# Kernel optimization log

Measured on AMD Instinct MI355X. Metric: run time of the kernel, lower is better.

Reference implementation:

```python
import jax, jax.numpy as jnp
import numpy as np

N_NODES = 50000

def _sage_conv(x, src, dst, W_l, b_l, W_r):
    # mean-aggregate neighbor features: messages x[src] summed into dst
    msgs = x[src]                                   # [E, d]
    agg = jax.ops.segment_sum(msgs, dst, num_segments=N_NODES)  # [N, d]
    ones = jnp.ones((src.shape[0],), dtype=x.dtype)
    cnt = jax.ops.segment_sum(ones, dst, num_segments=N_NODES)  # [N]
    agg = agg / jnp.maximum(cnt, 1.0)[:, None]
    return agg @ W_l + b_l + x @ W_r


def setup_inputs() -> dict:
    key = jax.random.key(0)
    ks = jax.random.split(key, 8)
    d_in, hid, out = 64, 128, 64
    x = jax.random.normal(ks[0], (N_NODES, d_in), dtype=jnp.float32)
    edge_index = jax.random.randint(ks[1], (2, 1600000), 0, N_NODES, dtype=jnp.int64)
    def w(k, a, b):
        return jax.random.normal(k, (a, b), dtype=jnp.float32) / np.sqrt(a)
    return {
        "x": x,
        "edge_index": edge_index,
        "W_l1": w(ks[2], d_in, hid), "b_l1": jnp.zeros((hid,), jnp.float32),
        "W_r1": w(ks[3], d_in, hid),
        "W_l2": w(ks[4], hid, hid), "b_l2": jnp.zeros((hid,), jnp.float32),
        "W_r2": w(ks[5], hid, hid),
        "W_out": w(ks[6], hid, out), "b_out": jnp.zeros((out,), jnp.float32),
    }


def reference(x, edge_index, W_l1, b_l1, W_r1, W_l2, b_l2, W_r2, W_out, b_out):
    src, dst = edge_index[0], edge_index[1]
    h = jax.nn.relu(_sage_conv(x, src, dst, W_l1, b_l1, W_r1))
    h = jax.nn.relu(_sage_conv(h, src, dst, W_l2, b_l2, W_r2))
    return h @ W_out + b_out
```

## Files before the change

### kernel.cpp

```cpp
#include <hip/hip_runtime.h>


typedef unsigned short ushort_t;
typedef unsigned int uint_t;
typedef unsigned char uchar_t;
typedef __attribute__((ext_vector_type(8))) short short8;
typedef __attribute__((ext_vector_type(8))) ushort_t ushort8;
typedef __attribute__((ext_vector_type(4))) float f32x4;

#define BKT_SHIFT 7
#define BKT_NODES 128
#define BKT_CAP   5120
#define EPB       4096
#define QSCALE    32.0f
#define QINV      0.03125f
#define XQSCALE   16.0f

__device__ inline ushort_t bf16_rne(float v) {
    uint_t u = __float_as_uint(v);
    u += 0x7fffu + ((u >> 16) & 1u);
    return (ushort_t)(u >> 16);
}
__device__ inline float bf16_to_f(ushort_t h) {
    return __uint_as_float((uint_t)h << 16);
}


struct WPack {
    const float* srcp[5];
    ushort_t* dstp[5];
    int K[5], N[5], beg[5], end[5];
};

__global__ __launch_bounds__(1024)
void k_work(const int* __restrict__ src, const int* __restrict__ dst,
            uint_t* __restrict__ pairs, int* __restrict__ bcnt, int E, int nbk,
            int bbl, const float* __restrict__ x, ushort_t* __restrict__ xh,
            ushort_t* __restrict__ xl, uchar_t* __restrict__ xq,
            int NS, WPack wp, int total) {
    int tid = threadIdx.x;
    if (blockIdx.x >= bbl) {
        int t = (blockIdx.x - bbl) * 1024 + tid;
        if (t < NS) {
            float v = x[t];
            ushort_t h = bf16_rne(v);
            xh[t] = h;
            xl[t] = bf16_rne(v - bf16_to_f(h));
            int qv = (int)(v * XQSCALE + 128.5f);
            qv = qv < 0 ? 0 : (qv > 255 ? 255 : qv);
            xq[t] = (uchar_t)qv;
            return;
        }
        t -= NS;
        if (t >= total) return;
#pragma unroll
        for (int m = 0; m < 5; ++m) {
            if (t >= wp.beg[m] && t < wp.end[m]) {
                int i = t - wp.beg[m];
                int K = wp.K[m], N = wp.N[m];
                int k = i / N, nn = i % N;
                int NT = N >> 4;
                int kt = k >> 5, bq = (k >> 3) & 3, j = k & 7;
                int nt = nn >> 4, lane = (bq << 4) | (nn & 15);
                int base = (((kt * NT + nt) << 6) + lane) * 8 + j;
                int halfsz = (K >> 5) * NT * 512;
                float v = wp.srcp[m][i];
                ushort_t h = bf16_rne(v);
                wp.dstp[m][base] = h;
                wp.dstp[m][halfsz + base] = bf16_rne(v - bf16_to_f(h));
            }
        }
        return;
    }

    __shared__ int h[4][512];
    int sub = tid & 3;
    for (int i = tid; i < 4 * 512; i += 1024) ((int*)h)[i] = 0;
    __syncthreads();

    int e = blockIdx.x * EPB + tid * 4;
    bool full = (e + 4 <= E);
    int4 d4 = {0, 0, 0, 0}, s4 = {0, 0, 0, 0};
    if (full) {
        d4 = *(const int4*)(dst + e);
        s4 = *(const int4*)(src + e);
        atomicAdd(&h[sub][d4.x >> BKT_SHIFT], 1);
        atomicAdd(&h[sub][d4.y >> BKT_SHIFT], 1);
        atomicAdd(&h[sub][d4.z >> BKT_SHIFT], 1);
        atomicAdd(&h[sub][d4.w >> BKT_SHIFT], 1);
    } else {
        for (int t = e; t < E && t < e + 4; ++t)
            atomicAdd(&h[sub][dst[t] >> BKT_SHIFT], 1);
    }
    __syncthreads();
    for (int i = tid; i < nbk; i += 1024) {
        int c0 = h[0][i], c1 = h[1][i], c2 = h[2][i], c3 = h[3][i];
        int c = c0 + c1 + c2 + c3;
        int bs = c ? atomicAdd(&bcnt[i], c) : 0;
        h[0][i] = bs; h[1][i] = bs + c0; h[2][i] = bs + c0 + c1;
        h[3][i] = bs + c0 + c1 + c2;
    }
    __syncthreads();
    if (full) {
        int dd[4] = {d4.x, d4.y, d4.z, d4.w};
        int ss[4] = {s4.x, s4.y, s4.z, s4.w};
#pragma unroll
        for (int t = 0; t < 4; ++t) {
            int b = dd[t] >> BKT_SHIFT;
            int r = atomicAdd(&h[sub][b], 1);
            pairs[(size_t)b * BKT_CAP + r] =
                (uint_t)(ss[t] & 0xFFFF) | ((uint_t)(dd[t] & (BKT_NODES - 1)) << 16);
        }
    } else {
        for (int t = e; t < E && t < e + 4; ++t) {
            int d = dst[t];
            int b = d >> BKT_SHIFT;
            int r = atomicAdd(&h[sub][b], 1);
            pairs[(size_t)b * BKT_CAP + r] =
                (uint_t)(src[t] & 0xFFFF) | ((uint_t)(d & (BKT_NODES - 1)) << 16);
        }
    }
}


__global__ __launch_bounds__(1024) void k_csr(const uint_t* __restrict__ pairs,
                                              const int* __restrict__ bcnt,
                                              int* __restrict__ off,
                                              ushort_t* __restrict__ col, int n) {
    __shared__ int hist[BKT_NODES];
    __shared__ int s[BKT_NODES];
    __shared__ int cur[BKT_NODES];
    __shared__ int bofs_s;
    int b = blockIdx.x, tid = threadIdx.x;
    if (tid < 64) {
        int p = 0;
        for (int i = tid; i < b; i += 64) p += bcnt[i];
#pragma unroll
        for (int m = 1; m < 64; m <<= 1) p += __shfl_xor(p, m);
        if (tid == 0) bofs_s = p;
    }
    if (tid < BKT_NODES) hist[tid] = 0;
    __syncthreads();
    int bofs = bofs_s;
    int cnt = bcnt[b];
    const uint_t* p = pairs + (size_t)b * BKT_CAP;
    for (int i = tid; i < cnt; i += 1024) atomicAdd(&hist[(p[i] >> 16) & 127], 1);
    __syncthreads();
    int v = (tid < BKT_NODES) ? hist[tid] : 0;
    if (tid < BKT_NODES) s[tid] = v;
    __syncthreads();
    for (int ofs = 1; ofs < BKT_NODES; ofs <<= 1) {
        int t = (tid >= ofs && tid < BKT_NODES) ? s[tid - ofs] : 0;
        __syncthreads();
        if (tid < BKT_NODES) s[tid] += t;
        __syncthreads();
    }
    if (tid < BKT_NODES) {
        int excl = bofs + s[tid] - v;
        int node = b * BKT_NODES + tid;
        if (node <= n) off[node] = excl;
        cur[tid] = excl;
    }
    __syncthreads();
    for (int i = tid; i < cnt; i += 1024) {
        uint_t pk = p[i];
        int pos = atomicAdd(&cur[(pk >> 16) & 127], 1);
        col[pos] = (ushort_t)(pk & 0xFFFF);
    }
}

template <int ROWB>
__device__ inline void gather_u8(const uchar_t* __restrict__ fbase,
                                 const ushort_t* __restrict__ col,
                                 int s0, int s1, int sub,
                                 uint_t (&ae)[4], uint_t (&ao)[4]) {
    constexpr int EPI = 1024 / ROWB;
#pragma unroll
    for (int i = 0; i < 4; ++i) { ae[i] = 0u; ao[i] = 0u; }
    int e = s0;
    for (; e + 4 * EPI <= s1; e += 4 * EPI) {
        int c[4];
        uint4 q[4];
#pragma unroll
        for (int j = 0; j < 4; ++j) c[j] = col[e + j * EPI + sub];
#pragma unroll
        for (int j = 0; j < 4; ++j) q[j] = *(const uint4*)(fbase + (size_t)c[j] * ROWB);
#pragma unroll
        for (int j = 0; j < 4; ++j) {
            const uint_t* u = (const uint_t*)&q[j];
#pragma unroll
            for (int i = 0; i < 4; ++i) {
                ae[i] += u[i] & 0x00FF00FFu;
                ao[i] += (u[i] >> 8) & 0x00FF00FFu;
            }
        }
    }
    for (; e < s1; e += 2 * EPI) {
        int last = s1 - 1;
        int c[2];
        uint_t msk[2];
        uint4 q[2];
#pragma unroll
        for (int j = 0; j < 2; ++j) {
            int idx = e + j * EPI + sub;
            msk[j] = (idx < s1) ? 0xFFFFFFFFu : 0u;
            c[j] = col[min(idx, last)];
        }
#pragma unroll
        for (int j = 0; j < 2; ++j) q[j] = *(const uint4*)(fbase + (size_t)c[j] * ROWB);
#pragma unroll
        for (int j = 0; j < 2; ++j) {
            const uint_t* u = (const uint_t*)&q[j];
#pragma unroll
            for (int i = 0; i < 4; ++i) {
                uint_t um = u[i] & msk[j];
                ae[i] += um & 0x00FF00FFu;
                ao[i] += (um >> 8) & 0x00FF00FFu;
            }
        }
    }
}

__device__ inline f32x4 mfma3(f32x4 acc, short8 ah, short8 al, short8 bh, short8 bl) {
    acc = __builtin_amdgcn_mfma_f32_16x16x32_bf16(ah, bh, acc, 0, 0, 0);
    acc = __builtin_amdgcn_mfma_f32_16x16x32_bf16(al, bh, acc, 0, 0, 0);
    acc = __builtin_amdgcn_mfma_f32_16x16x32_bf16(ah, bl, acc, 0, 0, 0);
    return acc;
}


__global__ __launch_bounds__(512)
void k_layer1(const uchar_t* __restrict__ xq, const ushort_t* __restrict__ xh,
              const ushort_t* __restrict__ xl,
              const int* __restrict__ off, const ushort_t* __restrict__ col,
              const ushort_t* __restrict__ Wlp, const ushort_t* __restrict__ Wrp,
              const float* __restrict__ bias, ushort_t* __restrict__ Oh,
              uchar_t* __restrict__ OqA, uchar_t* __restrict__ OqB, int n) {
    __shared__ ushort_t Ahs[32][72];
    __shared__ ushort_t Als[32][72];
    int tid = threadIdx.x, waveid = tid >> 6, lane = tid & 63;
    int base = blockIdx.x * 32;
    int li = lane & 3;
    int sub = lane >> 2;
    const uchar_t* fbase = xq + li * 16;

    for (int q = 0; q < 4; ++q) {
        int node = base + waveid * 4 + q;
        int nd = node < n ? node : n - 1;
        int s0 = off[nd], s1 = off[nd + 1];
        uint_t ae[4], ao[4];
        gather_u8<64>(fbase, col, s0, s1, sub, ae, ao);
#pragma unroll
        for (int m = 4; m < 64; m <<= 1) {
#pragma unroll
            for (int i = 0; i < 4; ++i) {
                ae[i] += __shfl_xor(ae[i], m);
                ao[i] += __shfl_xor(ao[i], m);
            }
        }
        if (sub == 0) {
            int deg = s1 - s0;
            float inv = 1.f / (XQSCALE * fmaxf((float)deg, 1.f));
            float c8 = deg > 0 ? 8.f : 0.f;
            ushort_t vh[16], vl[16];
#pragma unroll
            for (int i = 0; i < 4; ++i) {
                uint_t f[4] = {ae[i] & 0xFFFFu, ao[i] & 0xFFFFu,
                               ae[i] >> 16, ao[i] >> 16};
#pragma unroll
                for (int b = 0; b < 4; ++b) {
                    float mval = (float)f[b] * inv - c8;
                    ushort_t h = bf16_rne(mval);
                    vh[i * 4 + b] = h;
                    vl[i * 4 + b] = bf16_rne(mval - bf16_to_f(h));
                }
            }
            int r = waveid * 4 + q;
            *(ushort8*)&Ahs[r][li * 16] = *(ushort8*)&vh[0];
            *(ushort8*)&Ahs[r][li * 16 + 8] = *(ushort8*)&vh[8];
            *(ushort8*)&Als[r][li * 16] = *(ushort8*)&vl[0];
            *(ushort8*)&Als[r][li * 16 + 8] = *(ushort8*)&vl[8];
        }
    }
    __syncthreads();

    int rowt = waveid >> 2, c0 = waveid & 3;
    int colq = lane & 15, quad = lane >> 4;
    int arow = rowt * 16 + colq;
    short8 fah[2], fal[2], fxh[2], fxl[2];
#pragma unroll
    for (int kt = 0; kt < 2; ++kt) {
        fah[kt] = *(const short8*)&Ahs[arow][kt * 32 + quad * 8];
        fal[kt] = *(const short8*)&Als[arow][kt * 32 + quad * 8];
    }
    int grow = base + arow; if (grow >= n) grow = n - 1;
#pragma unroll
    for (int kt = 0; kt < 2; ++kt) {
        fxh[kt] = *(const short8*)(xh + (size_t)grow * 64 + kt * 32 + quad * 8);
        fxl[kt] = *(const short8*)(xl + (size_t)grow * 64 + kt * 32 + quad * 8);
    }
#pragma unroll
    for (int t = 0; t < 2; ++t) {
        int nt = c0 + t * 4;
        float bv = bias[nt * 16 + colq];
        f32x4 acc = (f32x4){bv, bv, bv, bv};
#pragma unroll
        for (int kt = 0; kt < 2; ++kt) {
            const ushort_t* pL = Wlp + ((size_t)((kt * 8 + nt) << 6) + lane) * 8;
            acc = mfma3(acc, fah[kt], fal[kt],
                        *(const short8*)pL, *(const short8*)(pL + 8192));
            const ushort_t* pR = Wrp + ((size_t)((kt * 8 + nt) << 6) + lane) * 8;
            acc = mfma3(acc, fxh[kt], fxl[kt],
                        *(const short8*)pR, *(const short8*)(pR + 8192));
        }
        int rowb = base + rowt * 16 + quad * 4;
        int cix = nt * 16 + colq;
        uchar_t* Oqh = t ? OqB : OqA;
        int qix = c0 * 16 + colq;
#pragma unroll
        for (int r = 0; r < 4; ++r) {
            int row = rowb + r;
            if (row < n) {
                float v = fmaxf(acc[r], 0.f);
                Oh[(size_t)row * 128 + cix] = bf16_rne(v);
                int qv = (int)(v * QSCALE + 0.5f);
                Oqh[(size_t)row * 64 + qix] = (uchar_t)(qv > 255 ? 255 : qv);
            }
        }
    }
}


__global__ __launch_bounds__(256)
void k_aggh(const uchar_t* __restrict__ fq, const int* __restrict__ off,
            const ushort_t* __restrict__ col, uint_t* __restrict__ S, int n) {
    int wave = (int)((blockIdx.x * (unsigned)blockDim.x + threadIdx.x) >> 6);
    int lane = threadIdx.x & 63;
    if (wave >= n) return;
    int li = lane & 3, sub = lane >> 2;
    int s0 = off[wave], s1 = off[wave + 1];
    uint_t ae[4], ao[4];
    gather_u8<64>(fq + li * 16, col, s0, s1, sub, ae, ao);
#pragma unroll
    for (int m = 4; m < 64; m <<= 1) {
#pragma unroll
        for (int i = 0; i < 4; ++i) {
            ae[i] += __shfl_xor(ae[i], m);
            ao[i] += __shfl_xor(ao[i], m);
        }
    }
    if (sub == 0) {
        uint4 va = {ae[0], ae[1], ae[2], ae[3]};
        uint4 vo = {ao[0], ao[1], ao[2], ao[3]};
        *(uint4*)(S + (size_t)wave * 32 + li * 8) = va;
        *(uint4*)(S + (size_t)wave * 32 + li * 8 + 4) = vo;
    }
}


#define L2R 136
__global__ __launch_bounds__(256)
void k_dense2(const uint_t* __restrict__ SA, const uint_t* __restrict__ SB,
              const int* __restrict__ off, const ushort_t* __restrict__ h1h,
              const ushort_t* __restrict__ Wlp, const ushort_t* __restrict__ Wrp,
              const float* __restrict__ b2, const ushort_t* __restrict__ Wop,
              const float* __restrict__ bo, float* __restrict__ out, int n) {
    __shared__ ushort_t Ah[16][L2R], Al[16][L2R];
    __shared__ ushort_t Hh[16][L2R], Hl[16][L2R];
    int tid = threadIdx.x, waveid = tid >> 6, lane = tid & 63;
    int base = blockIdx.x * 16;

    int j = lane & 31;
    const uint_t* Sp = (lane < 32) ? SA : SB;
    int fofs = (lane < 32) ? 0 : 64;
    int fl = fofs + ((j >> 3) << 4) + ((j & 3) << 2) + ((j >> 2) & 1);
    for (int q = 0; q < 4; ++q) {
        int node = base + waveid * 4 + q;
        int nd = node < n ? node : n - 1;
        float inv = QINV / fmaxf((float)(off[nd + 1] - off[nd]), 1.f);
        uint_t s = Sp[(size_t)nd * 32 + j];
        float v0 = (float)(s & 0xFFFFu) * inv;
        float v1 = (float)(s >> 16) * inv;
        ushort_t h0 = bf16_rne(v0), h1v = bf16_rne(v1);
        int row = waveid * 4 + q;
        Ah[row][fl] = h0;      Al[row][fl] = bf16_rne(v0 - bf16_to_f(h0));
        Ah[row][fl + 2] = h1v; Al[row][fl + 2] = bf16_rne(v1 - bf16_to_f(h1v));
    }
    __syncthreads();

    int colx = lane & 15, quad = lane >> 4;
    int arow = colx;
    int grow = base + arow; if (grow >= n) grow = n - 1;
    short8 gah[4], gal[4], sh[4];
#pragma unroll
    for (int kt = 0; kt < 4; ++kt) {
        gah[kt] = *(const short8*)&Ah[arow][kt * 32 + quad * 8];
        gal[kt] = *(const short8*)&Al[arow][kt * 32 + quad * 8];
        sh[kt]  = *(const short8*)(h1h + (size_t)grow * 128 + kt * 32 + quad * 8);
    }
#pragma unroll
    for (int t = 0; t < 2; ++t) {
        int nt = waveid + t * 4;
        float bv = b2[nt * 16 + colx];
        f32x4 acc = (f32x4){bv, bv, bv, bv};
#pragma unroll
        for (int kt = 0; kt < 4; ++kt) {
            const ushort_t* pL = Wlp + ((size_t)((kt * 8 + nt) << 6) + lane) * 8;
            acc = mfma3(acc, gah[kt], gal[kt],
                        *(const short8*)pL, *(const short8*)(pL + 16384));
            const ushort_t* pR = Wrp + ((size_t)((kt * 8 + nt) << 6) + lane) * 8;
            short8 bh = *(const short8*)pR;
            short8 bl = *(const short8*)(pR + 16384);
            acc = __builtin_amdgcn_mfma_f32_16x16x32_bf16(sh[kt], bh, acc, 0, 0, 0);
            acc = __builtin_amdgcn_mfma_f32_16x16x32_bf16(sh[kt], bl, acc, 0, 0, 0);
        }
#pragma unroll
        for (int r = 0; r < 4; ++r) {
            int row = quad * 4 + r;
            float v = fmaxf(acc[r], 0.f);
            ushort_t h = bf16_rne(v);
            Hh[row][nt * 16 + colx] = h;
            Hl[row][nt * 16 + colx] = bf16_rne(v - bf16_to_f(h));
        }
    }
    __syncthreads();

    short8 hh[4], hl[4];
#pragma unroll
    for (int kt = 0; kt < 4; ++kt) {
        hh[kt] = *(const short8*)&Hh[arow][kt * 32 + quad * 8];
        hl[kt] = *(const short8*)&Hl[arow][kt * 32 + quad * 8];
    }
    int nt2 = waveid;
    float bv = bo[nt2 * 16 + colx];
    f32x4 acc2 = (f32x4){bv, bv, bv, bv};
#pragma unroll
    for (int kt = 0; kt < 4; ++kt) {
        const ushort_t* p = Wop + ((size_t)((kt * 4 + nt2) << 6) + lane) * 8;
        acc2 = mfma3(acc2, hh[kt], hl[kt],
                     *(const short8*)p, *(const short8*)(p + 8192));
    }
#pragma unroll
    for (int r = 0; r < 4; ++r) {
        int row = base + quad * 4 + r;
        if (row < n) out[(size_t)row * 64 + nt2 * 16 + colx] = acc2[r];
    }
}


static inline size_t align256(size_t x) { return (x + 255) & ~(size_t)255; }

extern "C" void kernel_launch(void* const* d_in, const int* in_sizes, int n_in,
                              void* d_out, int out_size, void* d_ws, size_t ws_size,
                              hipStream_t stream) {
    const float* x   = (const float*)d_in[0];
    const int*   ei  = (const int*)d_in[1];
    const float* Wl1 = (const float*)d_in[2];
    const float* bl1 = (const float*)d_in[3];
    const float* Wr1 = (const float*)d_in[4];
    const float* Wl2 = (const float*)d_in[5];
    const float* bl2 = (const float*)d_in[6];
    const float* Wr2 = (const float*)d_in[7];
    const float* Wo  = (const float*)d_in[8];
    const float* bo  = (const float*)d_in[9];

    const int N = in_sizes[0] / 64;
    const int E = in_sizes[1] / 2;
    const int* src = ei;
    const int* dst = ei + E;
    const int nbk = (N + BKT_NODES - 1) >> BKT_SHIFT;

    char* ws = (char*)d_ws;
    int* off = (int*)ws;            ws += align256((size_t)(N + 1) * 4);
    int* bcnt = (int*)ws;           ws += align256((size_t)nbk * 4);
    uint_t* pairs = (uint_t*)ws;    ws += align256((size_t)nbk * BKT_CAP * 4);
    ushort_t* col = (ushort_t*)ws;  ws += align256((size_t)E * 2);
    ushort_t* xh  = (ushort_t*)ws;  ws += align256((size_t)N * 64 * 2);
    ushort_t* xl  = (ushort_t*)ws;  ws += align256((size_t)N * 64 * 2);
    uchar_t*  xq  = (uchar_t*)ws;   ws += align256((size_t)N * 64);
    ushort_t* h1h = (ushort_t*)ws;  ws += align256((size_t)N * 128 * 2);
    uchar_t*  h1qA = (uchar_t*)ws;  ws += align256((size_t)N * 64);
    uchar_t*  h1qB = (uchar_t*)ws;  ws += align256((size_t)N * 64);
    uint_t*   SA  = (uint_t*)ws;    ws += align256((size_t)N * 32 * 4);
    uint_t*   SB  = (uint_t*)ws;    ws += align256((size_t)N * 32 * 4);
    ushort_t* Wl1p = (ushort_t*)ws; ws += align256((size_t)2 * 64 * 128 * 2);
    ushort_t* Wr1p = (ushort_t*)ws; ws += align256((size_t)2 * 64 * 128 * 2);
    ushort_t* Wl2p = (ushort_t*)ws; ws += align256((size_t)2 * 128 * 128 * 2);
    ushort_t* Wr2p = (ushort_t*)ws; ws += align256((size_t)2 * 128 * 128 * 2);
    ushort_t* Wop  = (ushort_t*)ws; ws += align256((size_t)2 * 128 * 64 * 2);

    WPack wp;
    wp.srcp[0] = Wl1; wp.dstp[0] = Wl1p; wp.K[0] = 64;  wp.N[0] = 128;
    wp.srcp[1] = Wr1; wp.dstp[1] = Wr1p; wp.K[1] = 64;  wp.N[1] = 128;
    wp.srcp[2] = Wl2; wp.dstp[2] = Wl2p; wp.K[2] = 128; wp.N[2] = 128;
    wp.srcp[3] = Wr2; wp.dstp[3] = Wr2p; wp.K[3] = 128; wp.N[3] = 128;
    wp.srcp[4] = Wo;  wp.dstp[4] = Wop;  wp.K[4] = 128; wp.N[4] = 64;
    int acc_el = 0;
    for (int m = 0; m < 5; ++m) {
        wp.beg[m] = acc_el; acc_el += wp.K[m] * wp.N[m]; wp.end[m] = acc_el;
    }
    int NS = N * 64;

    hipMemsetAsync(bcnt, 0, (size_t)nbk * 4, stream);
    int bbl = (E + EPB - 1) / EPB;
    int pbl = (NS + acc_el + 1023) / 1024;
    k_work<<<bbl + pbl, 1024, 0, stream>>>(src, dst, pairs, bcnt, E, nbk, bbl,
                                           x, xh, xl, xq, NS, wp, acc_el);

    k_csr<<<nbk, 1024, 0, stream>>>(pairs, bcnt, off, col, N);

    k_layer1<<<(N + 31) / 32, 512, 0, stream>>>(xq, xh, xl, off, col, Wl1p,
                                                Wr1p, bl1, h1h, h1qA, h1qB, N);

    int aggbl = (N * 64 + 255) / 256;
    k_aggh<<<aggbl, 256, 0, stream>>>(h1qA, off, col, SA, N);
    k_aggh<<<aggbl, 256, 0, stream>>>(h1qB, off, col, SB, N);

    k_dense2<<<(N + 15) / 16, 256, 0, stream>>>(SA, SB, off, h1h, Wl2p, Wr2p,
                                                bl2, Wop, bo, (float*)d_out, N);
}
```

Measured before the change: 233.0 us.

## Replace CSR build with bucket-local LDS atomic aggregation fused into dense layers

Drops the CSR construction kernel and the separate per-node gather and aggregation kernels. Each 64-node bucket block now reads its unsorted (src,dst) pairs directly, accumulates quantized neighbor features into shared memory with atomics, then runs the dense MFMA stages in the same block. This cuts the launch count from six kernels to three and removes the off/col/SA/SB intermediate traffic. The cost is heavy LDS atomic contention and only about 782 blocks of 1024 threads, so occupancy may be low. Bucket capacity shrinks to 2816 edges per bucket, which risks overflow on skewed graphs.

After: 236.8 us. Within noise of the previous version (+1.6%).

```diff
diff --git a/kernel.cpp b/kernel.cpp
--- a/kernel.cpp
+++ b/kernel.cpp
@@ -8,9 +8,9 @@
 typedef __attribute__((ext_vector_type(8))) ushort_t ushort8;
 typedef __attribute__((ext_vector_type(4))) float f32x4;
 
-#define BKT_SHIFT 7
-#define BKT_NODES 128
-#define BKT_CAP   5120
+#define BKT_SHIFT 6
+#define BKT_NODES 64
+#define BKT_CAP   2816
 #define EPB       4096
 #define QSCALE    32.0f
 #define QINV      0.03125f
@@ -73,9 +73,9 @@
         return;
     }
 
-    __shared__ int h[4][512];
+    __shared__ int h[4][1024];
     int sub = tid & 3;
-    for (int i = tid; i < 4 * 512; i += 1024) ((int*)h)[i] = 0;
+    for (int i = tid; i < 4 * 1024; i += 1024) ((int*)h)[i] = 0;
     __syncthreads();
 
     int e = blockIdx.x * EPB + tid * 4;
@@ -122,105 +122,6 @@
     }
 }
 
-
-__global__ __launch_bounds__(1024) void k_csr(const uint_t* __restrict__ pairs,
-                                              const int* __restrict__ bcnt,
-                                              int* __restrict__ off,
-                                              ushort_t* __restrict__ col, int n) {
-    __shared__ int hist[BKT_NODES];
-    __shared__ int s[BKT_NODES];
-    __shared__ int cur[BKT_NODES];
-    __shared__ int bofs_s;
-    int b = blockIdx.x, tid = threadIdx.x;
-    if (tid < 64) {
-        int p = 0;
-        for (int i = tid; i < b; i += 64) p += bcnt[i];
-#pragma unroll
-        for (int m = 1; m < 64; m <<= 1) p += __shfl_xor(p, m);
-        if (tid == 0) bofs_s = p;
-    }
-    if (tid < BKT_NODES) hist[tid] = 0;
-    __syncthreads();
-    int bofs = bofs_s;
-    int cnt = bcnt[b];
-    const uint_t* p = pairs + (size_t)b * BKT_CAP;
-    for (int i = tid; i < cnt; i += 1024) atomicAdd(&hist[(p[i] >> 16) & 127], 1);
-    __syncthreads();
-    int v = (tid < BKT_NODES) ? hist[tid] : 0;
-    if (tid < BKT_NODES) s[tid] = v;
-    __syncthreads();
-    for (int ofs = 1; ofs < BKT_NODES; ofs <<= 1) {
-        int t = (tid >= ofs && tid < BKT_NODES) ? s[tid - ofs] : 0;
-        __syncthreads();
-        if (tid < BKT_NODES) s[tid] += t;
-        __syncthreads();
-    }
-    if (tid < BKT_NODES) {
-        int excl = bofs + s[tid] - v;
-        int node = b * BKT_NODES + tid;
-        if (node <= n) off[node] = excl;
-        cur[tid] = excl;
-    }
-    __syncthreads();
-    for (int i = tid; i < cnt; i += 1024) {
-        uint_t pk = p[i];
-        int pos = atomicAdd(&cur[(pk >> 16) & 127], 1);
-        col[pos] = (ushort_t)(pk & 0xFFFF);
-    }
-}
-
-template <int ROWB>
-__device__ inline void gather_u8(const uchar_t* __restrict__ fbase,
-                                 const ushort_t* __restrict__ col,
-                                 int s0, int s1, int sub,
-                                 uint_t (&ae)[4], uint_t (&ao)[4]) {
-    constexpr int EPI = 1024 / ROWB;
-#pragma unroll
-    for (int i = 0; i < 4; ++i) { ae[i] = 0u; ao[i] = 0u; }
-    int e = s0;
-    for (; e + 4 * EPI <= s1; e += 4 * EPI) {
-        int c[4];
-        uint4 q[4];
-#pragma unroll
-        for (int j = 0; j < 4; ++j) c[j] = col[e + j * EPI + sub];
-#pragma unroll
-        for (int j = 0; j < 4; ++j) q[j] = *(const uint4*)(fbase + (size_t)c[j] * ROWB);
-#pragma unroll
-        for (int j = 0; j < 4; ++j) {
-            const uint_t* u = (const uint_t*)&q[j];
-#pragma unroll
-            for (int i = 0; i < 4; ++i) {
-                ae[i] += u[i] & 0x00FF00FFu;
-                ao[i] += (u[i] >> 8) & 0x00FF00FFu;
-            }
-        }
-    }
-    for (; e < s1; e += 2 * EPI) {
-        int last = s1 - 1;
-        int c[2];
-        uint_t msk[2];
-        uint4 q[2];
-#pragma unroll
-        for (int j = 0; j < 2; ++j) {
-            int idx = e + j * EPI + sub;
-            msk[j] = (idx < s1) ? 0xFFFFFFFFu : 0u;
-            c[j] = col[min(idx, last)];
-        }
-#pragma unroll
-        for (int j = 0; j < 2; ++j) q[j] = *(const uint4*)(fbase + (size_t)c[j] * ROWB);
-#pragma unroll
-        for (int j = 0; j < 2; ++j) {
-            const uint_t* u = (const uint_t*)&q[j];
-#pragma unroll
-            for (int i = 0; i < 4; ++i) {
-                uint_t um = u[i] & msk[j];
-                ae[i] += um & 0x00FF00FFu;
-                ao[i] += (um >> 8) & 0x00FF00FFu;
-            }
-        }
-    }
-}
-
 __device__ inline f32x4 mfma3(f32x4 acc, short8 ah, short8 al, short8 bh, short8 bl) {
     acc = __builtin_amdgcn_mfma_f32_16x16x32_bf16(ah, bh, acc, 0, 0, 0);
     acc = __builtin_amdgcn_mfma_f32_16x16x32_bf16(al, bh, acc, 0, 0, 0);
@@ -228,63 +129,82 @@
     return acc;
 }
 
-
-__global__ __launch_bounds__(512)
-void k_layer1(const uchar_t* __restrict__ xq, const ushort_t* __restrict__ xh,
-              const ushort_t* __restrict__ xl,
-              const int* __restrict__ off, const ushort_t* __restrict__ col,
-              const ushort_t* __restrict__ Wlp, const ushort_t* __restrict__ Wrp,
-              const float* __restrict__ bias, ushort_t* __restrict__ Oh,
-              uchar_t* __restrict__ OqA, uchar_t* __restrict__ OqB, int n) {
-    __shared__ ushort_t Ahs[32][72];
-    __shared__ ushort_t Als[32][72];
-    int tid = threadIdx.x, waveid = tid >> 6, lane = tid & 63;
-    int base = blockIdx.x * 32;
-    int li = lane & 3;
-    int sub = lane >> 2;
-    const uchar_t* fbase = xq + li * 16;
-
-    for (int q = 0; q < 4; ++q) {
-        int node = base + waveid * 4 + q;
-        int nd = node < n ? node : n - 1;
-        int s0 = off[nd], s1 = off[nd + 1];
-        uint_t ae[4], ao[4];
-        gather_u8<64>(fbase, col, s0, s1, sub, ae, ao);
-#pragma unroll
-        for (int m = 4; m < 64; m <<= 1) {
-#pragma unroll
-            for (int i = 0; i < 4; ++i) {
-                ae[i] += __shfl_xor(ae[i], m);
-                ao[i] += __shfl_xor(ao[i], m);
+__device__ inline void unpack2(uint_t v, uint_t& a, uint_t& b) {
+    a = (v & 0xFFu) | ((v << 8) & 0x00FF0000u);
+    b = ((v >> 16) & 0xFFu) | ((v >> 8) & 0x00FF0000u);
+}
+
+
+__global__ __launch_bounds__(1024)
+void k_push1(const uchar_t* __restrict__ xq, const ushort_t* __restrict__ xh,
+             const ushort_t* __restrict__ xl, const uint_t* __restrict__ pairs,
+             const int* __restrict__ bcnt,
+             const ushort_t* __restrict__ Wlp, const ushort_t* __restrict__ Wrp,
+             const float* __restrict__ bias, ushort_t* __restrict__ Oh,
+             uchar_t* __restrict__ OqA, uchar_t* __restrict__ OqB, int n) {
+    __shared__ uint_t accs[64][33];
+    __shared__ int cnt[64];
+    __shared__ ushort_t Ahs[64][72];
+    __shared__ ushort_t Als[64][72];
+    int tid = threadIdx.x;
+    int b = blockIdx.x, base = b * 64;
+    for (int i = tid; i < 64 * 33; i += 1024) ((uint_t*)accs)[i] = 0;
+    if (tid < 64) cnt[tid] = 0;
+    __syncthreads();
+
+    int ecnt = bcnt[b];
+    const uint_t* pb = pairs + (size_t)b * BKT_CAP;
+    int li = tid & 3, grp = tid >> 2;
+    for (int e = grp; e < ecnt; e += 512) {
+        uint_t pk0 = pb[e];
+        int e1 = e + 256;
+        bool v1 = e1 < ecnt;
+        uint_t pk1 = pb[v1 ? e1 : e];
+        int c0 = pk0 & 0xFFFF, d0 = (pk0 >> 16) & 63;
+        int c1 = pk1 & 0xFFFF, d1 = (pk1 >> 16) & 63;
+        uint4 q0 = *(const uint4*)(xq + (size_t)c0 * 64 + li * 16);
+        uint4 q1 = *(const uint4*)(xq + (size_t)c1 * 64 + li * 16);
+        const uint_t* u0 = (const uint_t*)&q0;
+#pragma unroll
+        for (int k = 0; k < 4; ++k) {
+            uint_t a, bb;
+            unpack2(u0[k], a, bb);
+            atomicAdd(&accs[d0][li * 8 + 2 * k], a);
+            atomicAdd(&accs[d0][li * 8 + 2 * k + 1], bb);
+        }
+        if (li == 0) atomicAdd(&cnt[d0], 1);
+        if (v1) {
+            const uint_t* u1 = (const uint_t*)&q1;
+#pragma unroll
+            for (int k = 0; k < 4; ++k) {
+                uint_t a, bb;
+                unpack2(u1[k], a, bb);
+                atomicAdd(&accs[d1][li * 8 + 2 * k], a);
+                atomicAdd(&accs[d1][li * 8 + 2 * k + 1], bb);
             }
-        }
-        if (sub == 0) {
-            int deg = s1 - s0;
-            float inv = 1.f / (XQSCALE * fmaxf((float)deg, 1.f));
-            float c8 = deg > 0 ? 8.f : 0.f;
-            ushort_t vh[16], vl[16];
-#pragma unroll
-            for (int i = 0; i < 4; ++i) {
-                uint_t f[4] = {ae[i] & 0xFFFFu, ao[i] & 0xFFFFu,
-                               ae[i] >> 16, ao[i] >> 16};
-#pragma unroll
-                for (int b = 0; b < 4; ++b) {
-                    float mval = (float)f[b] * inv - c8;
-                    ushort_t h = bf16_rne(mval);
-                    vh[i * 4 + b] = h;
-                    vl[i * 4 + b] = bf16_rne(mval - bf16_to_f(h));
-                }
-            }
-            int r = waveid * 4 + q;
-            *(ushort8*)&Ahs[r][li * 16] = *(ushort8*)&vh[0];
-            *(ushort8*)&Ahs[r][li * 16 + 8] = *(ushort8*)&vh[8];
-            *(ushort8*)&Als[r][li * 16] = *(ushort8*)&vl[0];
-            *(ushort8*)&Als[r][li * 16 + 8] = *(ushort8*)&vl[8];
-        }
-    }
-    __syncthreads();
-
-    int rowt = waveid >> 2, c0 = waveid & 3;
+            if (li == 0) atomicAdd(&cnt[d1], 1);
+        }
+    }
+    __syncthreads();
+
+    for (int idx = tid; idx < 64 * 32; idx += 1024) {
+        int node = idx >> 5, j = idx & 31;
+        int deg = cnt[node];
+        float inv = 1.f / (XQSCALE * fmaxf((float)deg, 1.f));
+        float c8 = deg > 0 ? 8.f : 0.f;
+        uint_t s = accs[node][j];
+        float v0 = (float)(s & 0xFFFFu) * inv - c8;
+        float v1 = (float)(s >> 16) * inv - c8;
+        ushort_t h0 = bf16_rne(v0), h1v = bf16_rne(v1);
+        *(uint_t*)&Ahs[node][2 * j] = (uint_t)h0 | ((uint_t)h1v << 16);
+        ushort_t l0 = bf16_rne(v0 - bf16_to_f(h0));
+        ushort_t l1 = bf16_rne(v1 - bf16_to_f(h1v));
+        *(uint_t*)&Als[node][2 * j] = (uint_t)l0 | ((uint_t)l1 << 16);
+    }
+    __syncthreads();
+
+    int waveid = tid >> 6, lane = tid & 63;
+    int rowt = waveid >> 2, c0w = waveid & 3;
     int colq = lane & 15, quad = lane >> 4;
     int arow = rowt * 16 + colq;
     short8 fah[2], fal[2], fxh[2], fxl[2];
@@ -301,7 +221,7 @@
     }
 #pragma unroll
     for (int t = 0; t < 2; ++t) {
-        int nt = c0 + t * 4;
+        int nt = c0w + t * 4;
         float bv = bias[nt * 16 + colq];
         f32x4 acc = (f32x4){bv, bv, bv, bv};
 #pragma unroll
@@ -316,7 +236,7 @@
         int rowb = base + rowt * 16 + quad * 4;
         int cix = nt * 16 + colq;
         uchar_t* Oqh = t ? OqB : OqA;
-        int qix = c0 * 16 + colq;
+        int qix = c0w * 16 + colq;
 #pragma unroll
         for (int r = 0; r < 4; ++r) {
             int row = rowb + r;
@@ -331,65 +251,81 @@
 }
 
 
-__global__ __launch_bounds__(256)
-void k_aggh(const uchar_t* __restrict__ fq, const int* __restrict__ off,
-            const ushort_t* __restrict__ col, uint_t* __restrict__ S, int n) {
-    int wave = (int)((blockIdx.x * (unsigned)blockDim.x + threadIdx.x) >> 6);
-    int lane = threadIdx.x & 63;
-    if (wave >= n) return;
-    int li = lane & 3, sub = lane >> 2;
-    int s0 = off[wave], s1 = off[wave + 1];
-    uint_t ae[4], ao[4];
-    gather_u8<64>(fq + li * 16, col, s0, s1, sub, ae, ao);
-#pragma unroll
-    for (int m = 4; m < 64; m <<= 1) {
-#pragma unroll
-        for (int i = 0; i < 4; ++i) {
-            ae[i] += __shfl_xor(ae[i], m);
-            ao[i] += __shfl_xor(ao[i], m);
-        }
-    }
-    if (sub == 0) {
-        uint4 va = {ae[0], ae[1], ae[2], ae[3]};
-        uint4 vo = {ao[0], ao[1], ao[2], ao[3]};
-        *(uint4*)(S + (size_t)wave * 32 + li * 8) = va;
-        *(uint4*)(S + (size_t)wave * 32 + li * 8 + 4) = vo;
-    }
-}
-
-
-#define L2R 136
-__global__ __launch_bounds__(256)
-void k_dense2(const uint_t* __restrict__ SA, const uint_t* __restrict__ SB,
-              const int* __restrict__ off, const ushort_t* __restrict__ h1h,
-              const ushort_t* __restrict__ Wlp, const ushort_t* __restrict__ Wrp,
-              const float* __restrict__ b2, const ushort_t* __restrict__ Wop,
-              const float* __restrict__ bo, float* __restrict__ out, int n) {
-    __shared__ ushort_t Ah[16][L2R], Al[16][L2R];
-    __shared__ ushort_t Hh[16][L2R], Hl[16][L2R];
-    int tid = threadIdx.x, waveid = tid >> 6, lane = tid & 63;
-    int base = blockIdx.x * 16;
-
-    int j = lane & 31;
-    const uint_t* Sp = (lane < 32) ? SA : SB;
-    int fofs = (lane < 32) ? 0 : 64;
-    int fl = fofs + ((j >> 3) << 4) + ((j & 3) << 2) + ((j >> 2) & 1);
-    for (int q = 0; q < 4; ++q) {
-        int node = base + waveid * 4 + q;
-        int nd = node < n ? node : n - 1;
-        float inv = QINV / fmaxf((float)(off[nd + 1] - off[nd]), 1.f);
-        uint_t s = Sp[(size_t)nd * 32 + j];
+__global__ __launch_bounds__(1024)
+void k_push2(const uchar_t* __restrict__ h1qA, const uchar_t* __restrict__ h1qB,
+             const uint_t* __restrict__ pairs, const int* __restrict__ bcnt,
+             const ushort_t* __restrict__ h1h,
+             const ushort_t* __restrict__ Wlp, const ushort_t* __restrict__ Wrp,
+             const float* __restrict__ b2, const ushort_t* __restrict__ Wop,
+             const float* __restrict__ bo, float* __restrict__ out, int n) {
+    __shared__ uint_t accs[64][65];
+    __shared__ int cnt[64];
+    __shared__ ushort_t Ah[64][136];
+    __shared__ ushort_t Al[64][136];
+    int tid = threadIdx.x;
+    int b = blockIdx.x, base = b * 64;
+    for (int i = tid; i < 64 * 65; i += 1024) ((uint_t*)accs)[i] = 0;
+    if (tid < 64) cnt[tid] = 0;
+    __syncthreads();
+
+    int ecnt = bcnt[b];
+    const uint_t* pb = pairs + (size_t)b * BKT_CAP;
+    int li = tid & 3, grp = tid >> 2;
+#pragma unroll
+    for (int pass = 0; pass < 2; ++pass) {
+        const uchar_t* tab = pass ? h1qB : h1qA;
+        int jofs = pass ? 32 : 0;
+        for (int e = grp; e < ecnt; e += 512) {
+            uint_t pk0 = pb[e];
+            int e1 = e + 256;
+            bool v1 = e1 < ecnt;
+            uint_t pk1 = pb[v1 ? e1 : e];
+            int c0 = pk0 & 0xFFFF, d0 = (pk0 >> 16) & 63;
+            int c1 = pk1 & 0xFFFF, d1 = (pk1 >> 16) & 63;
+            uint4 q0 = *(const uint4*)(tab + (size_t)c0 * 64 + li * 16);
+            uint4 q1 = *(const uint4*)(tab + (size_t)c1 * 64 + li * 16);
+            const uint_t* u0 = (const uint_t*)&q0;
+#pragma unroll
+            for (int k = 0; k < 4; ++k) {
+                uint_t a, bb;
+                unpack2(u0[k], a, bb);
+                atomicAdd(&accs[d0][jofs + li * 8 + 2 * k], a);
+                atomicAdd(&accs[d0][jofs + li * 8 + 2 * k + 1], bb);
+            }
+            if (pass == 0 && li == 0) atomicAdd(&cnt[d0], 1);
+            if (v1) {
+                const uint_t* u1 = (const uint_t*)&q1;
+#pragma unroll
+                for (int k = 0; k < 4; ++k) {
+                    uint_t a, bb;
+                    unpack2(u1[k], a, bb);
+                    atomicAdd(&accs[d1][jofs + li * 8 + 2 * k], a);
+                    atomicAdd(&accs[d1][jofs + li * 8 + 2 * k + 1], bb);
+                }
+                if (pass == 0 && li == 0) atomicAdd(&cnt[d1], 1);
+            }
+        }
+    }
+    __syncthreads();
+
+    for (int idx = tid; idx < 64 * 64; idx += 1024) {
+        int node = idx >> 6, j = idx & 63;
+        float inv = QINV / fmaxf((float)cnt[node], 1.f);
+        uint_t s = accs[node][j];
         float v0 = (float)(s & 0xFFFFu) * inv;
         float v1 = (float)(s >> 16) * inv;
         ushort_t h0 = bf16_rne(v0), h1v = bf16_rne(v1);
-        int row = waveid * 4 + q;
-        Ah[row][fl] = h0;      Al[row][fl] = bf16_rne(v0 - bf16_to_f(h0));
-        Ah[row][fl + 2] = h1v; Al[row][fl + 2] = bf16_rne(v1 - bf16_to_f(h1v));
-    }
-    __syncthreads();
-
+        *(uint_t*)&Ah[node][2 * j] = (uint_t)h0 | ((uint_t)h1v << 16);
+        ushort_t l0 = bf16_rne(v0 - bf16_to_f(h0));
+        ushort_t l1 = bf16_rne(v1 - bf16_to_f(h1v));
+        *(uint_t*)&Al[node][2 * j] = (uint_t)l0 | ((uint_t)l1 << 16);
+    }
+    __syncthreads();
+
+    int waveid = tid >> 6, lane = tid & 63;
+    int rowt = waveid >> 2, c0w = waveid & 3;
     int colx = lane & 15, quad = lane >> 4;
-    int arow = colx;
+    int arow = rowt * 16 + colx;
     int grow = base + arow; if (grow >= n) grow = n - 1;
     short8 gah[4], gal[4], sh[4];
 #pragma unroll
@@ -398,9 +334,12 @@
         gal[kt] = *(const short8*)&Al[arow][kt * 32 + quad * 8];
         sh[kt]  = *(const short8*)(h1h + (size_t)grow * 128 + kt * 32 + quad * 8);
     }
+    __syncthreads();
+
+    f32x4 accd[2];
 #pragma unroll
     for (int t = 0; t < 2; ++t) {
-        int nt = waveid + t * 4;
+        int nt = c0w + t * 4;
         float bv = b2[nt * 16 + colx];
         f32x4 acc = (f32x4){bv, bv, bv, bv};
 #pragma unroll
@@ -414,24 +353,30 @@
             acc = __builtin_amdgcn_mfma_f32_16x16x32_bf16(sh[kt], bh, acc, 0, 0, 0);
             acc = __builtin_amdgcn_mfma_f32_16x16x32_bf16(sh[kt], bl, acc, 0, 0, 0);
         }
+        accd[t] = acc;
+    }
+#pragma unroll
+    for (int t = 0; t < 2; ++t) {
+        int nt = c0w + t * 4;
 #pragma unroll
         for (int r = 0; r < 4; ++r) {
-            int row = quad * 4 + r;
-            float v = fmaxf(acc[r], 0.f);
+            int row = rowt * 16 + quad * 4 + r;
+            float v = fmaxf(accd[t][r], 0.f);
             ushort_t h = bf16_rne(v);
-            Hh[row][nt * 16 + colx] = h;
-            Hl[row][nt * 16 + colx] = bf16_rne(v - bf16_to_f(h));
-        }
-    }
-    __syncthreads();
-
+            Ah[row][nt * 16 + colx] = h;
+            Al[row][nt * 16 + colx] = bf16_rne(v - bf16_to_f(h));
+        }
+    }
+    __syncthreads();
+
+    int rowt2 = waveid >> 2, nt2 = waveid & 3;
+    int arow2 = rowt2 * 16 + colx;
     short8 hh[4], hl[4];
 #pragma unroll
     for (int kt = 0; kt < 4; ++kt) {
-        hh[kt] = *(const short8*)&Hh[arow][kt * 32 + quad * 8];
-        hl[kt] = *(const short8*)&Hl[arow][kt * 32 + quad * 8];
-    }
-    int nt2 = waveid;
+        hh[kt] = *(const short8*)&Ah[arow2][kt * 32 + quad * 8];
+        hl[kt] = *(const short8*)&Al[arow2][kt * 32 + quad * 8];
+    }
     float bv = bo[nt2 * 16 + colx];
     f32x4 acc2 = (f32x4){bv, bv, bv, bv};
 #pragma unroll
@@ -442,7 +387,7 @@
     }
 #pragma unroll
     for (int r = 0; r < 4; ++r) {
-        int row = base + quad * 4 + r;
+        int row = base + rowt2 * 16 + quad * 4 + r;
         if (row < n) out[(size_t)row * 64 + nt2 * 16 + colx] = acc2[r];
     }
 }
@@ -471,18 +416,14 @@
     const int nbk = (N + BKT_NODES - 1) >> BKT_SHIFT;
 
     char* ws = (char*)d_ws;
-    int* off = (int*)ws;            ws += align256((size_t)(N + 1) * 4);
     int* bcnt = (int*)ws;           ws += align256((size_t)nbk * 4);
     uint_t* pairs = (uint_t*)ws;    ws += align256((size_t)nbk * BKT_CAP * 4);
-    ushort_t* col = (ushort_t*)ws;  ws += align256((size_t)E * 2);
     ushort_t* xh  = (ushort_t*)ws;  ws += align256((size_t)N * 64 * 2);
     ushort_t* xl  = (ushort_t*)ws;  ws += align256((size_t)N * 64 * 2);
     uchar_t*  xq  = (uchar_t*)ws;   ws += align256((size_t)N * 64);
     ushort_t* h1h = (ushort_t*)ws;  ws += align256((size_t)N * 128 * 2);
     uchar_t*  h1qA = (uchar_t*)ws;  ws += align256((size_t)N * 64);
     uchar_t*  h1qB = (uchar_t*)ws;  ws += align256((size_t)N * 64);
-    uint_t*   SA  = (uint_t*)ws;    ws += align256((size_t)N * 32 * 4);
-    uint_t*   SB  = (uint_t*)ws;    ws += align256((size_t)N * 32 * 4);
     ushort_t* Wl1p = (ushort_t*)ws; ws += align256((size_t)2 * 64 * 128 * 2);
     ushort_t* Wr1p = (ushort_t*)ws; ws += align256((size_t)2 * 64 * 128 * 2);
     ushort_t* Wl2p = (ushort_t*)ws; ws += align256((size_t)2 * 128 * 128 * 2);
@@ -507,15 +448,9 @@
     k_work<<<bbl + pbl, 1024, 0, stream>>>(src, dst, pairs, bcnt, E, nbk, bbl,
                                            x, xh, xl, xq, NS, wp, acc_el);
 
-    k_csr<<<nbk, 1024, 0, stream>>>(pairs, bcnt, off, col, N);
-
-    k_layer1<<<(N + 31) / 32, 512, 0, stream>>>(xq, xh, xl, off, col, Wl1p,
-                                                Wr1p, bl1, h1h, h1qA, h1qB, N);
-
-    int aggbl = (N * 64 + 255) / 256;
-    k_aggh<<<aggbl, 256, 0, stream>>>(h1qA, off, col, SA, N);
-    k_aggh<<<aggbl, 256, 0, stream>>>(h1qB, off, col, SB, N);
-
-    k_dense2<<<(N + 15) / 16, 256, 0, stream>>>(SA, SB, off, h1h, Wl2p, Wr2p,
-                                                bl2, Wop, bo, (float*)d_out, N);
-}
+    k_push1<<<nbk, 1024, 0, stream>>>(xq, xh, xl, pairs, bcnt, Wl1p, Wr1p,
+                                      bl1, h1h, h1qA, h1qB, N);
+
+    k_push2<<<nbk, 1024, 0, stream>>>(h1qA, h1qB, pairs, bcnt, h1h, Wl2p,
+                                      Wr2p, bl2, Wop, bo, (float*)d_out, N);
+}
```
